# Kernel optimization log

Hardware: AMD Instinct MI355X
Metric: run time of the kernel (lower is better)

Reference implementation:

```python
import jax, jax.numpy as jnp
import numpy as np

B, L, D, NID = 256, 512, 64, 10000


def _count_appearances(src_ids, dst_ids):
    # Equivalent to per-sample unique+bincount: for each position i,
    # count occurrences of that id in the src sequence and in the dst sequence.
    # src_ids, dst_ids: (B, L) int64. Padding id == 0 is masked to 0 afterward.
    src_in_src = (src_ids[:, :, None] == src_ids[:, None, :]).sum(-1)  # (B, L)
    src_in_dst = (src_ids[:, :, None] == dst_ids[:, None, :]).sum(-1)
    dst_in_src = (dst_ids[:, :, None] == src_ids[:, None, :]).sum(-1)
    dst_in_dst = (dst_ids[:, :, None] == dst_ids[:, None, :]).sum(-1)
    src_app = jnp.stack([src_in_src, src_in_dst], axis=-1).astype(jnp.float32)  # (B, L, 2)
    dst_app = jnp.stack([dst_in_src, dst_in_dst], axis=-1).astype(jnp.float32)
    src_app = jnp.where((src_ids == 0)[..., None], 0.0, src_app)
    dst_app = jnp.where((dst_ids == 0)[..., None], 0.0, dst_app)
    return src_app, dst_app


def _encode(app, W1, b1, W2, b2):
    # app: (B, L, 2) -> unsqueeze(-1) -> Linear(1->D) -> ReLU -> Linear(D->D) -> sum over channel dim 2
    h = jax.nn.relu(app[..., None] * W1[:, 0] + b1)          # (B, L, 2, D)
    out = jnp.einsum('blcd,ed->blce', h, W2) + b2             # (B, L, 2, D)
    return out.sum(axis=2)                                    # (B, L, D)


def setup_inputs() -> dict:
    key = jax.random.key(0)
    k1, k2, k3, k4, k5, k6 = jax.random.split(key, 6)
    return {
        'src_ids': jax.random.randint(k1, (B, L), 0, NID, dtype=jnp.int64) if jax.config.read('jax_enable_x64') else jax.random.randint(k1, (B, L), 0, NID).astype(jnp.int32),
        'dst_ids': jax.random.randint(k2, (B, L), 0, NID).astype(jnp.int32),
        'W1': jax.random.normal(k3, (D, 1), dtype=jnp.float32) * 0.5,
        'b1': jax.random.normal(k4, (D,), dtype=jnp.float32) * 0.1,
        'W2': jax.random.normal(k5, (D, D), dtype=jnp.float32) * (1.0 / np.sqrt(D)),
        'b2': jax.random.normal(k6, (D,), dtype=jnp.float32) * 0.1,
    }


def reference(src_ids, dst_ids, W1, b1, W2, b2):
    src_app, dst_app = _count_appearances(src_ids, dst_ids)
    src_feat = _encode(src_app, W1, b1, W2, b2)
    dst_feat = _encode(dst_app, W1, b1, W2, b2)
    return src_feat, dst_feat
```

## Files before the change

### kernel.cpp

```cpp
#include <hip/hip_runtime.h>

#define BB  256
#define LL  512
#define DD  64
#define NID 10000
#define NW  (NID / 2)
#define NROWS (2 * BB * LL)
#define NT4  (NROWS * 16)

__global__ __launch_bounds__(256) void build_table(
    const float* __restrict__ W1, const float* __restrict__ b1,
    const float* __restrict__ W2, const float* __restrict__ b2,
    float* __restrict__ T)
{
    __shared__ float w2l[DD][DD + 1];
    __shared__ float hsh[4][DD];
    const int t = threadIdx.x;
    const int w = t >> 6;
    const int e = t & 63;
    for (int i = t; i < DD * DD; i += 256)
        w2l[i >> 6][i & 63] = W2[i];
    const int a = blockIdx.x * 4 + w;
    hsh[w][e] = fmaxf((float)a * W1[e] + b1[e], 0.0f);
    __syncthreads();
    if (a <= LL) {
        float acc = b2[e];
#pragma unroll
        for (int d = 0; d < DD; ++d)
            acc = fmaf(hsh[w][d], w2l[e][d], acc);
        T[a * DD + e] = acc;
    }
}

__global__ __launch_bounds__(512) void count_rows(
    const int* __restrict__ src_ids, const int* __restrict__ dst_ids,
    unsigned int* __restrict__ R)
{
    __shared__ unsigned int hs[NW];
    __shared__ unsigned int hd[NW];
    const int t = threadIdx.x;
    const int b = blockIdx.x;

    uint4* z1 = (uint4*)hs;
    uint4* z2 = (uint4*)hd;
    const uint4 z = make_uint4(0u, 0u, 0u, 0u);
    for (int i = t; i < NW / 4; i += 512) { z1[i] = z; z2[i] = z; }
    const int sid = src_ids[b * LL + t];
    const int did = dst_ids[b * LL + t];
    __syncthreads();

    atomicAdd(&hs[sid >> 1], 1u << ((sid & 1) * 16));
    atomicAdd(&hd[did >> 1], 1u << ((did & 1) * 16));
    __syncthreads();

    unsigned int c_ss = (hs[sid >> 1] >> ((sid & 1) * 16)) & 0xFFFFu;
    unsigned int c_sd = (hd[sid >> 1] >> ((sid & 1) * 16)) & 0xFFFFu;
    unsigned int c_ds = (hs[did >> 1] >> ((did & 1) * 16)) & 0xFFFFu;
    unsigned int c_dd = (hd[did >> 1] >> ((did & 1) * 16)) & 0xFFFFu;
    if (sid == 0) { c_ss = 0u; c_sd = 0u; }
    if (did == 0) { c_ds = 0u; c_dd = 0u; }
    R[b * LL + t]           = c_ss | (c_sd << 16);
    R[BB * LL + b * LL + t] = c_ds | (c_dd << 16);
}

__global__ __launch_bounds__(256) void stream_out(
    const unsigned int* __restrict__ R, const float* __restrict__ T,
    float4* __restrict__ out4)
{
    const float4* T4 = (const float4*)T;
    int g = blockIdx.x * 256 + threadIdx.x;
    const int stride = gridDim.x * 256;
    for (; g < NT4; g += stride) {
        const unsigned int r = R[g >> 4];
        const int q = g & 15;
        const float4 x = T4[(r & 0xFFFFu) * 16 + q];
        const float4 y = T4[(r >> 16) * 16 + q];
        float4 v;
        v.x = x.x + y.x; v.y = x.y + y.y; v.z = x.z + y.z; v.w = x.w + y.w;
        out4[g] = v;
    }
}

extern "C" void kernel_launch(void* const* d_in, const int* in_sizes, int n_in,
                              void* d_out, int out_size, void* d_ws, size_t ws_size,
                              hipStream_t stream) {
    const int*   src_ids = (const int*)d_in[0];
    const int*   dst_ids = (const int*)d_in[1];
    const float* W1      = (const float*)d_in[2];
    const float* b1      = (const float*)d_in[3];
    const float* W2      = (const float*)d_in[4];
    const float* b2      = (const float*)d_in[5];

    float*        T = (float*)d_ws;
    unsigned int* R = (unsigned int*)((char*)d_ws + (256 << 10));

    build_table<<<dim3(129), dim3(256), 0, stream>>>(W1, b1, W2, b2, T);
    count_rows<<<dim3(BB), dim3(512), 0, stream>>>(src_ids, dst_ids, R);
    stream_out<<<dim3(2048), dim3(256), 0, stream>>>(R, T, (float4*)d_out);
}
```

Baseline: 94.19 us.

## Fuse histogram counting with output streaming into one per-batch kernel

Merges the count_rows and stream_out kernels into one kernel with one 1024-thread block per batch row. Each block builds the shared-memory histograms, keeps the packed counts in LDS, and then writes that row's output directly from the table. This removes the intermediate R buffer round trip through global memory and one kernel launch. In exchange the output write uses only 256 blocks, each with large LDS use (about 48KB), so fewer waves may be in flight to hide memory latency than with the old 2048-block streaming grid.

```diff
diff --git a/kernel.cpp b/kernel.cpp
--- a/kernel.cpp
+++ b/kernel.cpp
@@ -5,8 +5,6 @@
 #define DD  64
 #define NID 10000
 #define NW  (NID / 2)
-#define NROWS (2 * BB * LL)
-#define NT4  (NROWS * 16)
 
 __global__ __launch_bounds__(256) void build_table(
     const float* __restrict__ W1, const float* __restrict__ b1,
@@ -32,52 +30,62 @@
     }
 }
 
-__global__ __launch_bounds__(512) void count_rows(
+__global__ __launch_bounds__(1024) void count_stream(
     const int* __restrict__ src_ids, const int* __restrict__ dst_ids,
-    unsigned int* __restrict__ R)
+    const float* __restrict__ T, float4* __restrict__ out4)
 {
     __shared__ unsigned int hs[NW];
     __shared__ unsigned int hd[NW];
+    __shared__ int ids[2 * LL];
+    __shared__ unsigned int cnt[2 * LL];
+
     const int t = threadIdx.x;
     const int b = blockIdx.x;
 
     uint4* z1 = (uint4*)hs;
     uint4* z2 = (uint4*)hd;
     const uint4 z = make_uint4(0u, 0u, 0u, 0u);
-    for (int i = t; i < NW / 4; i += 512) { z1[i] = z; z2[i] = z; }
-    const int sid = src_ids[b * LL + t];
-    const int did = dst_ids[b * LL + t];
+    for (int i = t; i < NW / 4; i += 1024) { z1[i] = z; z2[i] = z; }
+
+    ids[t] = (t < LL) ? src_ids[b * LL + t] : dst_ids[b * LL + (t - LL)];
     __syncthreads();
 
-    atomicAdd(&hs[sid >> 1], 1u << ((sid & 1) * 16));
-    atomicAdd(&hd[did >> 1], 1u << ((did & 1) * 16));
+    const int id = ids[t];
+    unsigned int* h = (t < LL) ? hs : hd;
+    atomicAdd(&h[id >> 1], 1u << ((id & 1) * 16));
     __syncthreads();
 
-    unsigned int c_ss = (hs[sid >> 1] >> ((sid & 1) * 16)) & 0xFFFFu;
-    unsigned int c_sd = (hd[sid >> 1] >> ((sid & 1) * 16)) & 0xFFFFu;
-    unsigned int c_ds = (hs[did >> 1] >> ((did & 1) * 16)) & 0xFFFFu;
-    unsigned int c_dd = (hd[did >> 1] >> ((did & 1) * 16)) & 0xFFFFu;
-    if (sid == 0) { c_ss = 0u; c_sd = 0u; }
-    if (did == 0) { c_ds = 0u; c_dd = 0u; }
-    R[b * LL + t]           = c_ss | (c_sd << 16);
-    R[BB * LL + b * LL + t] = c_ds | (c_dd << 16);
-}
+    unsigned int c0 = (hs[id >> 1] >> ((id & 1) * 16)) & 0xFFFFu;
+    unsigned int c1 = (hd[id >> 1] >> ((id & 1) * 16)) & 0xFFFFu;
+    if (id == 0) { c0 = 0u; c1 = 0u; }
+    cnt[t] = c0 | (c1 << 16);
+    __syncthreads();
 
-__global__ __launch_bounds__(256) void stream_out(
-    const unsigned int* __restrict__ R, const float* __restrict__ T,
-    float4* __restrict__ out4)
-{
     const float4* T4 = (const float4*)T;
-    int g = blockIdx.x * 256 + threadIdx.x;
-    const int stride = gridDim.x * 256;
-    for (; g < NT4; g += stride) {
-        const unsigned int r = R[g >> 4];
-        const int q = g & 15;
-        const float4 x = T4[(r & 0xFFFFu) * 16 + q];
-        const float4 y = T4[(r >> 16) * 16 + q];
+    const int q     = t & 15;
+    const int rbase = t >> 4;
+    float4* osrc = out4 + (size_t)b * LL * 16;
+    float4* odst = out4 + (size_t)BB * LL * 16 + (size_t)b * LL * 16;
+
+#pragma unroll 4
+    for (int pass = 0; pass < 8; ++pass) {
+        const int r = pass * 64 + rbase;
+        const unsigned int c = cnt[r];
+        const float4 x = T4[(c & 0xFFFFu) * 16 + q];
+        const float4 y = T4[(c >> 16) * 16 + q];
         float4 v;
         v.x = x.x + y.x; v.y = x.y + y.y; v.z = x.z + y.z; v.w = x.w + y.w;
-        out4[g] = v;
+        osrc[r * 16 + q] = v;
+    }
+#pragma unroll 4
+    for (int pass = 8; pass < 16; ++pass) {
+        const int r = pass * 64 + rbase;
+        const unsigned int c = cnt[r];
+        const float4 x = T4[(c & 0xFFFFu) * 16 + q];
+        const float4 y = T4[(c >> 16) * 16 + q];
+        float4 v;
+        v.x = x.x + y.x; v.y = x.y + y.y; v.z = x.z + y.z; v.w = x.w + y.w;
+        odst[(r - LL) * 16 + q] = v;
     }
 }
 
@@ -91,10 +99,8 @@
     const float* W2      = (const float*)d_in[4];
     const float* b2      = (const float*)d_in[5];
 
-    float*        T = (float*)d_ws;
-    unsigned int* R = (unsigned int*)((char*)d_ws + (256 << 10));
+    float* T = (float*)d_ws;
 
     build_table<<<dim3(129), dim3(256), 0, stream>>>(W1, b1, W2, b2, T);
-    count_rows<<<dim3(BB), dim3(512), 0, stream>>>(src_ids, dst_ids, R);
-    stream_out<<<dim3(2048), dim3(256), 0, stream>>>(R, T, (float4*)d_out);
+    count_stream<<<dim3(BB), dim3(1024), 0, stream>>>(src_ids, dst_ids, T, (float4*)d_out);
 }
```

After: 91.20 us. 1.03x faster.
